# Kernel tuning notes

Hardware: AMD Instinct MI355X
Metric: run time of the kernel (lower is better)

Reference implementation:

```python
import jax, jax.numpy as jnp
import numpy as np

IOU_THRESHOLD = 0.5  # default in ObjectUtils.nms
N_BOXES = 10000


def setup_inputs() -> dict:
    key = jax.random.key(0)
    k1, k2 = jax.random.split(key)
    boxes = jax.random.uniform(k1, (N_BOXES, 4), dtype=jnp.float32)  # normalized cxcywh
    scores = jax.random.uniform(k2, (N_BOXES,), dtype=jnp.float32)
    return {"boxes_cxcywh": boxes, "scores": scores}


def _cxcywh_to_ltrb(b):
    cx, cy, w, h = b[:, 0], b[:, 1], b[:, 2], b[:, 3]
    return jnp.stack([cx - w / 2, cy - h / 2, cx + w / 2, cy + h / 2], axis=1)


def _pairwise_iou(a, b):
    # a: [N1,4] ltrb, b: [N2,4] ltrb -> [N1,N2] (matches ObjectUtils.compute_iou)
    lt = jnp.maximum(a[:, None, :2], b[None, :, :2])
    rb = jnp.minimum(a[:, None, 2:], b[None, :, 2:])
    wh = jnp.clip(rb - lt, 0.0)
    inter = wh[..., 0] * wh[..., 1]
    area_a = (a[:, 2] - a[:, 0]) * (a[:, 3] - a[:, 1])
    area_b = (b[:, 2] - b[:, 0]) * (b[:, 3] - b[:, 1])
    return inter / (area_a[:, None] + area_b[None, :] - inter)


def reference(boxes_cxcywh, scores):
    ltrb = _cxcywh_to_ltrb(boxes_cxcywh)
    iou = _pairwise_iou(ltrb, ltrb)  # [N,N]

    # ---- greedy NMS, faithful to ObjectUtils.nms (unclamped intersection,
    # retain when iou < threshold) expressed as a jit-friendly suppression loop ----
    n = ltrb.shape[0]
    order = jnp.argsort(-scores)  # highest score first (torch.sort ascending, pop last)
    bs = ltrb[order]
    l, t, r, b = bs[:, 0], bs[:, 1], bs[:, 2], bs[:, 3]
    area = (r - l) * (b - t)
    inter_nms = (jnp.minimum(r[:, None], r[None, :]) - jnp.maximum(l[:, None], l[None, :])) * \
                (jnp.minimum(b[:, None], b[None, :]) - jnp.maximum(t[:, None], t[None, :]))
    iou_nms = inter_nms / (area[:, None] + area[None, :] - inter_nms)
    ar = jnp.arange(n)

    def body(i, keep):
        # box i (in sorted order) suppresses lower-scored boxes only if it is itself kept
        suppress = keep[i] & (iou_nms[i] >= IOU_THRESHOLD) & (ar > i)
        return keep & jnp.logical_not(suppress)

    keep_sorted = jax.lax.fori_loop(0, n, body, jnp.ones((n,), dtype=bool))
    keep = jnp.zeros((n,), dtype=bool).at[order].set(keep_sorted)
    return iou, keep
```

## Files before the change

kernel.cpp:

```cpp
#include <hip/hip_runtime.h>

typedef unsigned long long u64;

#define THR 0.5f

__device__ __forceinline__ void conv_box(const float4 b, float& l, float& t,
                                         float& r, float& bo, float& a) {
  #pragma clang fp contract(off)
  float hw = 0.5f * b.z;
  float hh = 0.5f * b.w;
  l = b.x - hw;
  t = b.y - hh;
  r = b.x + hw;
  bo = b.y + hh;
  a = (r - l) * (bo - t);
}

__global__ void k_zero(int* __restrict__ rank, int n) {
  int i = blockIdx.x * blockDim.x + threadIdx.x;
  if (i < n) rank[i] = 0;
}

__global__ void k_rank(const float* __restrict__ scores, int* __restrict__ rank,
                       int n, int jchunk) {
  int i = blockIdx.x * blockDim.x + threadIdx.x;
  if (i >= n) return;
  float si = scores[i];
  int j0 = blockIdx.y * jchunk;
  int j1 = min(j0 + jchunk, n);
  int c = 0;
  for (int j = j0; j < j1; ++j) {
    float sj = scores[j];
    c += ((sj > si) || (sj == si && j < i)) ? 1 : 0;
  }
  if (c) atomicAdd(rank + i, c);
}

__global__ void k_scatter(const float4* __restrict__ boxes, const int* __restrict__ rank,
                          float* __restrict__ sl, float* __restrict__ st,
                          float* __restrict__ sr, float* __restrict__ sb,
                          float* __restrict__ sa, int* __restrict__ sidx, int n) {
  int i = blockIdx.x * blockDim.x + threadIdx.x;
  if (i >= n) return;
  float l, t, r, b, a;
  conv_box(boxes[i], l, t, r, b, a);
  int k = rank[i];
  sl[k] = l; st[k] = t; sr[k] = r; sb[k] = b; sa[k] = a; sidx[k] = i;
}

__global__ void k_mask(const float* __restrict__ sl, const float* __restrict__ st,
                       const float* __restrict__ sr, const float* __restrict__ sb,
                       const float* __restrict__ sa,
                       u64* __restrict__ mask, u64* __restrict__ diag,
                       u64* __restrict__ band, int n, int wstride) {
  #pragma clang fp contract(off)
  int k = blockIdx.x * blockDim.x + threadIdx.x;
  if (k >= n) return;
  int w = blockIdx.y;
  int jbase = w << 6;
  u64 word = 0;
  if (jbase + 63 > k) {
    float l = sl[k], t = st[k], r = sr[k], b = sb[k], a = sa[k];
    int jend = min(jbase + 64, n);
    for (int j = max(jbase, k + 1); j < jend; ++j) {
      float lmax = fmaxf(l, sl[j]);
      float tmax = fmaxf(t, st[j]);
      float rmin = fminf(r, sr[j]);
      float bmin = fminf(b, sb[j]);
      float wd = rmin - lmax;
      float hd = bmin - tmax;
      float inter = wd * hd;
      float denom = (a + sa[j]) - inter;
      float q = inter / denom;
      if (q >= THR) word |= 1ull << (j - jbase);
    }
  }
  mask[(size_t)k * wstride + w] = word;
  int kg = k >> 6;
  if (kg == w) diag[k] = word;
  if (w == kg + 1) band[k] = word;
}

__device__ __forceinline__ void scan_body6(
    const u64* __restrict__ mask, const u64* __restrict__ diag,
    const u64* __restrict__ band, const int* __restrict__ sidx,
    float* __restrict__ keep, int n, int wstride,
    u64* rem, u64* dsh, u64* bsh, int (*kept)[64], int* nk_sh) {
  int t = threadIdx.x, wv = t >> 6, lane = t & 63;
  int ng = (n + 63) >> 6;
  rem[t] = 0;
  if (t < 2) nk_sh[t] = 0;
  int scur = 0;
  u64 bnd = 0;
  if (wv == 0) {
    dsh[lane] = diag[lane];
    bsh[lane] = band[lane];
    if (lane < n) scur = sidx[lane];
  }
  __syncthreads();
  for (int g = 0; g < ng; ++g) {
    int base = g << 6;
    if (wv == 0) {
      int nxt = base + 64 + lane;
      u64 dnext = (g + 1 < ng) ? diag[nxt] : 0;
      u64 bnext = (g + 1 < ng) ? band[nxt] : 0;
      int snew = (g + 1 < ng && nxt < n) ? sidx[nxt] : 0;
      u64 s = rem[g] | bnd;
      int valid = n - base;
      if (valid < 64) s |= (~0ull) << valid;
      u64 kw = 0;
      #pragma unroll
      for (int c = 0; c < 8; ++c) {
        int b0 = c << 3;
        u64 e0 = dsh[b0 + 0], e1 = dsh[b0 + 1], e2 = dsh[b0 + 2], e3 = dsh[b0 + 3];
        u64 e4 = dsh[b0 + 4], e5 = dsh[b0 + 5], e6 = dsh[b0 + 6], e7 = dsh[b0 + 7];
        if ((unsigned)((s >> b0) & 0xFFull) != 0xFFu) {
          #define STEP(Q, EQ) if (!((s >> (b0 + Q)) & 1ull)) { kw |= 1ull << (b0 + Q); s |= EQ; }
          STEP(0, e0) STEP(1, e1) STEP(2, e2) STEP(3, e3)
          STEP(4, e4) STEP(5, e5) STEP(6, e6) STEP(7, e7)
          #undef STEP
        }
      }
      if (base + lane < n)
        keep[scur] = ((kw >> lane) & 1ull) ? 1.0f : 0.0f;
      int nk = __popcll(kw);
      if ((kw >> lane) & 1ull) {
        int pos = __popcll(kw & ((1ull << lane) - 1ull));
        kept[g & 1][pos] = lane;
      }
      int npad = (nk + 15) & ~15;
      if (lane >= nk && lane < npad) kept[g & 1][lane] = 0;
      if (lane == 0) nk_sh[g & 1] = nk;
      u64 bv = ((kw >> lane) & 1ull) ? bsh[lane] : 0ull;
      bv |= __shfl_xor(bv, 32);
      bv |= __shfl_xor(bv, 16);
      bv |= __shfl_xor(bv, 8);
      bv |= __shfl_xor(bv, 4);
      bv |= __shfl_xor(bv, 2);
      bv |= __shfl_xor(bv, 1);
      bnd = bv;
      dsh[lane] = dnext;
      bsh[lane] = bnext;
      scur = snew;
    } else {
      int w = t - 64;
      int gp = g - 1;
      if (gp >= 0 && w > g && w < ng) {
        int nkp = nk_sh[gp & 1];
        if (nkp) {
          const int* kp = kept[gp & 1];
          int basep = gp << 6;
          u64 acc = 0;
          for (int i = 0; i < nkp; i += 16) {
            int k0 = kp[i+0],  k1 = kp[i+1],  k2 = kp[i+2],  k3 = kp[i+3];
            int k4 = kp[i+4],  k5 = kp[i+5],  k6 = kp[i+6],  k7 = kp[i+7];
            int k8 = kp[i+8],  k9 = kp[i+9],  k10 = kp[i+10], k11 = kp[i+11];
            int k12 = kp[i+12], k13 = kp[i+13], k14 = kp[i+14], k15 = kp[i+15];
            u64 v0 = mask[(size_t)(basep + k0) * wstride + w];
            u64 v1 = mask[(size_t)(basep + k1) * wstride + w];
            u64 v2 = mask[(size_t)(basep + k2) * wstride + w];
            u64 v3 = mask[(size_t)(basep + k3) * wstride + w];
            u64 v4 = mask[(size_t)(basep + k4) * wstride + w];
            u64 v5 = mask[(size_t)(basep + k5) * wstride + w];
            u64 v6 = mask[(size_t)(basep + k6) * wstride + w];
            u64 v7 = mask[(size_t)(basep + k7) * wstride + w];
            u64 v8 = mask[(size_t)(basep + k8) * wstride + w];
            u64 v9 = mask[(size_t)(basep + k9) * wstride + w];
            u64 v10 = mask[(size_t)(basep + k10) * wstride + w];
            u64 v11 = mask[(size_t)(basep + k11) * wstride + w];
            u64 v12 = mask[(size_t)(basep + k12) * wstride + w];
            u64 v13 = mask[(size_t)(basep + k13) * wstride + w];
            u64 v14 = mask[(size_t)(basep + k14) * wstride + w];
            u64 v15 = mask[(size_t)(basep + k15) * wstride + w];
            acc |= v0;
            if (i + 1 < nkp)  acc |= v1;
            if (i + 2 < nkp)  acc |= v2;
            if (i + 3 < nkp)  acc |= v3;
            if (i + 4 < nkp)  acc |= v4;
            if (i + 5 < nkp)  acc |= v5;
            if (i + 6 < nkp)  acc |= v6;
            if (i + 7 < nkp)  acc |= v7;
            if (i + 8 < nkp)  acc |= v8;
            if (i + 9 < nkp)  acc |= v9;
            if (i + 10 < nkp) acc |= v10;
            if (i + 11 < nkp) acc |= v11;
            if (i + 12 < nkp) acc |= v12;
            if (i + 13 < nkp) acc |= v13;
            if (i + 14 < nkp) acc |= v14;
            if (i + 15 < nkp) acc |= v15;
          }
          rem[w] |= acc;
        }
      }
    }
    __syncthreads();
  }
}

__global__ __launch_bounds__(256, 1) void k_scan2(const u64* __restrict__ mask,
                                                  const u64* __restrict__ diag,
                                                  const u64* __restrict__ band,
                                                  const int* __restrict__ sidx,
                                                  float* __restrict__ keep,
                                                  int n, int wstride) {
  __shared__ u64 rem[256];
  __shared__ u64 dsh[64];
  __shared__ u64 bsh[64];
  __shared__ int kept[2][64];
  __shared__ int nk_sh[2];
  scan_body6(mask, diag, band, sidx, keep, n, wstride, rem, dsh, bsh, kept, nk_sh);
}

__device__ __forceinline__ float iou_one(float li, float ti, float ri, float bi, float ai,
                                         float lj, float tj, float rj, float bj, float aj) {
  float lmax = fmaxf(li, lj);
  float tmax = fmaxf(ti, tj);
  float rmin = fminf(ri, rj);
  float bmin = fminf(bi, bj);
  float w = fmaxf(rmin - lmax, 0.0f);
  float h = fmaxf(bmin - tmax, 0.0f);
  float inter = w * h;
  float denom = (ai + aj) - inter;
  return inter * __builtin_amdgcn_rcpf(denom);
}

__device__ __forceinline__ void iou_body(const float4* __restrict__ boxes,
                                         float* __restrict__ out,
                                         int n, int rpb, int bx, int by) {
  int nj4 = (n + 3) >> 2;
  int j4 = bx * 256 + threadIdx.x;
  if (j4 >= nj4) return;
  int j = j4 << 2;
  int jc1 = min(j + 1, n - 1), jc2 = min(j + 2, n - 1), jc3 = min(j + 3, n - 1);
  float l0,t0,r0,b0,a0, l1,t1,r1,b1,a1, l2,t2,r2,b2,a2, l3,t3,r3,b3,a3;
  conv_box(boxes[j],   l0,t0,r0,b0,a0);
  conv_box(boxes[jc1], l1,t1,r1,b1,a1);
  conv_box(boxes[jc2], l2,t2,r2,b2,a2);
  conv_box(boxes[jc3], l3,t3,r3,b3,a3);
  bool full = (j + 3) < n;
  for (int rr = 0; rr < rpb; ++rr) {
    int i = by * rpb + rr;
    if (i >= n) return;
    float li,ti,ri,bi,ai;
    conv_box(boxes[i], li,ti,ri,bi,ai);
    float4 o;
    o.x = iou_one(li,ti,ri,bi,ai, l0,t0,r0,b0,a0);
    o.y = iou_one(li,ti,ri,bi,ai, l1,t1,r1,b1,a1);
    o.z = iou_one(li,ti,ri,bi,ai, l2,t2,r2,b2,a2);
    o.w = iou_one(li,ti,ri,bi,ai, l3,t3,r3,b3,a3);
    size_t row = (size_t)i * n;
    if (full) {
      *reinterpret_cast<float4*>(out + row + j) = o;
    } else {
      out[row + j] = o.x;
      if (j + 1 < n) out[row + j + 1] = o.y;
      if (j + 2 < n) out[row + j + 2] = o.z;
    }
  }
}

__global__ void k_iou(const float4* __restrict__ boxes, float* __restrict__ out,
                      int n, int rpb) {
  iou_body(boxes, out, n, rpb, blockIdx.x, blockIdx.y);
}

__global__ __launch_bounds__(256) void k_fused(const float4* __restrict__ boxes,
                                               float* __restrict__ out,
                                               const u64* __restrict__ mask,
                                               const u64* __restrict__ diag,
                                               const u64* __restrict__ band,
                                               const int* __restrict__ sidx,
                                               float* __restrict__ keep,
                                               int n, int wstride, int rpb, int gx) {
  __shared__ u64 rem[256];
  __shared__ u64 dsh[64];
  __shared__ u64 bsh[64];
  __shared__ int kept[2][64];
  __shared__ int nk_sh[2];
  if (blockIdx.x == 0) {
    scan_body6(mask, diag, band, sidx, keep, n, wstride, rem, dsh, bsh, kept, nk_sh);
    return;
  }
  int id = blockIdx.x - 1;
  iou_body(boxes, out, n, rpb, id % gx, id / gx);
}

extern "C" void kernel_launch(void* const* d_in, const int* in_sizes, int n_in,
                              void* d_out, int out_size, void* d_ws, size_t ws_size,
                              hipStream_t stream) {
  const float* boxes = (const float*)d_in[0];
  const float* scores = (const float*)d_in[1];
  int n = in_sizes[1];
  float* out = (float*)d_out;
  size_t NN = (size_t)n * (size_t)n;
  float* keep = out + NN;

  int words = (n + 63) >> 6;
  int wstride = (words + 3) & ~3;
  size_t need = (size_t)n * wstride * 8
              + (size_t)words * 64 * 8 * 2
              + 256
              + (size_t)n * 4 * 7;
  bool use_ws = (ws_size >= need);

  char* base = use_ws ? (char*)d_ws : (char*)d_out;
  size_t off = 0;
  u64* mask = (u64*)(base + off); off += (size_t)n * wstride * 8;
  u64* diag = (u64*)(base + off); off += (size_t)words * 64 * 8;
  u64* band = (u64*)(base + off); off += (size_t)words * 64 * 8;
  off = (off + 255) & ~(size_t)255;
  float* sl  = (float*)(base + off); off += (size_t)n * 4;
  float* st_ = (float*)(base + off); off += (size_t)n * 4;
  float* sr  = (float*)(base + off); off += (size_t)n * 4;
  float* sb  = (float*)(base + off); off += (size_t)n * 4;
  float* sa  = (float*)(base + off); off += (size_t)n * 4;
  int* sidx  = (int*)(base + off); off += (size_t)n * 4;
  int* rank  = (int*)(base + off); off += (size_t)n * 4;

  int nb = (n + 255) / 256;
  k_zero<<<nb, 256, 0, stream>>>(rank, n);

  int jblocks = 40;
  int jchunk = (n + jblocks - 1) / jblocks;
  k_rank<<<dim3(nb, jblocks), 256, 0, stream>>>(scores, rank, n, jchunk);

  k_scatter<<<nb, 256, 0, stream>>>((const float4*)boxes, rank, sl, st_, sr, sb, sa, sidx, n);

  k_mask<<<dim3(nb, words), 256, 0, stream>>>(sl, st_, sr, sb, sa, mask, diag, band, n, wstride);

  int rpb = 10;
  int nj4 = (n + 3) >> 2;
  int gx = (nj4 + 255) / 256;
  int gy = (n + rpb - 1) / rpb;

  if (use_ws) {
    k_fused<<<gx * gy + 1, 256, 0, stream>>>((const float4*)boxes, out, mask, diag,
                                             band, sidx, keep, n, wstride, rpb, gx);
  } else {
    k_scan2<<<1, 256, 0, stream>>>(mask, diag, band, sidx, keep, n, wstride);
    k_iou<<<dim3(gx, gy), 256, 0, stream>>>((const float4*)boxes, out, n, rpb);
  }
}
```

Before: 383.2 us.

## Fuse rank/scatter kernels and streamline serial NMS scan inner loop

Merges the zero, rank and scatter kernels into a single kernel that counts rank over float4-vectorised scores without atomics, which removes two launches but leaves only 40 blocks each doing a full 10000-element sweep. The serial scan now preloads diagonal words from LDS into registers with double buffering, replaces the shuffle OR-reduction with DPP row operations plus readlane, and defers the keep-flag writes to a parallel pass at the end using a shared kwords array. The fused kernel also gets a launch bound hint of 4 blocks per CU. The kwords array is fixed at 160 entries, which caps n at 10240.

After: 717.2 us. +87.2%, slower.

```diff
diff --git a/kernel.cpp b/kernel.cpp
--- a/kernel.cpp
+++ b/kernel.cpp
@@ -16,36 +16,32 @@
   a = (r - l) * (bo - t);
 }
 
-__global__ void k_zero(int* __restrict__ rank, int n) {
-  int i = blockIdx.x * blockDim.x + threadIdx.x;
-  if (i < n) rank[i] = 0;
-}
-
-__global__ void k_rank(const float* __restrict__ scores, int* __restrict__ rank,
-                       int n, int jchunk) {
+__global__ void k_rankscatter(const float4* __restrict__ boxes,
+                              const float* __restrict__ scores,
+                              float* __restrict__ sl, float* __restrict__ st,
+                              float* __restrict__ sr, float* __restrict__ sb,
+                              float* __restrict__ sa, int* __restrict__ sidx, int n) {
   int i = blockIdx.x * blockDim.x + threadIdx.x;
   if (i >= n) return;
   float si = scores[i];
-  int j0 = blockIdx.y * jchunk;
-  int j1 = min(j0 + jchunk, n);
+  const float4* s4 = (const float4*)scores;
+  int n4 = n >> 2;
   int c = 0;
-  for (int j = j0; j < j1; ++j) {
+  for (int j4 = 0; j4 < n4; ++j4) {
+    float4 v = s4[j4];
+    int j = j4 << 2;
+    c += (v.x > si || (v.x == si && j + 0 < i)) ? 1 : 0;
+    c += (v.y > si || (v.y == si && j + 1 < i)) ? 1 : 0;
+    c += (v.z > si || (v.z == si && j + 2 < i)) ? 1 : 0;
+    c += (v.w > si || (v.w == si && j + 3 < i)) ? 1 : 0;
+  }
+  for (int j = n4 << 2; j < n; ++j) {
     float sj = scores[j];
-    c += ((sj > si) || (sj == si && j < i)) ? 1 : 0;
-  }
-  if (c) atomicAdd(rank + i, c);
-}
-
-__global__ void k_scatter(const float4* __restrict__ boxes, const int* __restrict__ rank,
-                          float* __restrict__ sl, float* __restrict__ st,
-                          float* __restrict__ sr, float* __restrict__ sb,
-                          float* __restrict__ sa, int* __restrict__ sidx, int n) {
-  int i = blockIdx.x * blockDim.x + threadIdx.x;
-  if (i >= n) return;
+    c += (sj > si || (sj == si && j < i)) ? 1 : 0;
+  }
   float l, t, r, b, a;
   conv_box(boxes[i], l, t, r, b, a);
-  int k = rank[i];
-  sl[k] = l; st[k] = t; sr[k] = r; sb[k] = b; sa[k] = a; sidx[k] = i;
+  sl[c] = l; st[c] = t; sr[c] = r; sb[c] = b; sa[c] = a; sidx[c] = i;
 }
 
 __global__ void k_mask(const float* __restrict__ sl, const float* __restrict__ st,
@@ -81,21 +77,40 @@
   if (w == kg + 1) band[k] = word;
 }
 
-__device__ __forceinline__ void scan_body6(
+__device__ __forceinline__ u64 wave_or_u64(u64 v) {
+  unsigned lo = (unsigned)v, hi = (unsigned)(v >> 32);
+#define DPP_OR(x, ctrl, rmask) \
+  x |= (unsigned)__builtin_amdgcn_update_dpp(0, (int)(x), ctrl, rmask, 0xF, true)
+  DPP_OR(lo, 0x111, 0xF); DPP_OR(hi, 0x111, 0xF);
+  DPP_OR(lo, 0x112, 0xF); DPP_OR(hi, 0x112, 0xF);
+  DPP_OR(lo, 0x114, 0xF); DPP_OR(hi, 0x114, 0xF);
+  DPP_OR(lo, 0x118, 0xF); DPP_OR(hi, 0x118, 0xF);
+  DPP_OR(lo, 0x142, 0xA); DPP_OR(hi, 0x142, 0xA);
+  DPP_OR(lo, 0x143, 0xC); DPP_OR(hi, 0x143, 0xC);
+#undef DPP_OR
+  unsigned flo = (unsigned)__builtin_amdgcn_readlane((int)lo, 63);
+  unsigned fhi = (unsigned)__builtin_amdgcn_readlane((int)hi, 63);
+  return ((u64)fhi << 32) | flo;
+}
+
+__device__ __forceinline__ void scan_body7(
     const u64* __restrict__ mask, const u64* __restrict__ diag,
     const u64* __restrict__ band, const int* __restrict__ sidx,
     float* __restrict__ keep, int n, int wstride,
-    u64* rem, u64* dsh, u64* bsh, int (*kept)[64], int* nk_sh) {
+    u64* rem, u64* dsh, u64* bsh, u64* kwords, int (*kept)[64], int* nk_sh) {
   int t = threadIdx.x, wv = t >> 6, lane = t & 63;
   int ng = (n + 63) >> 6;
   rem[t] = 0;
   if (t < 2) nk_sh[t] = 0;
-  int scur = 0;
   u64 bnd = 0;
+  u64 x0 = 0, x1 = 0, x2 = 0, x3 = 0, x4 = 0, x5 = 0, x6 = 0, x7 = 0;
+  const ulonglong2* d2 = (const ulonglong2*)dsh;
   if (wv == 0) {
     dsh[lane] = diag[lane];
     bsh[lane] = band[lane];
-    if (lane < n) scur = sidx[lane];
+    ulonglong2 p0 = d2[0], p1 = d2[1], p2 = d2[2], p3 = d2[3];
+    x0 = p0.x; x1 = p0.y; x2 = p1.x; x3 = p1.y;
+    x4 = p2.x; x5 = p2.y; x6 = p3.x; x7 = p3.y;
   }
   __syncthreads();
   for (int g = 0; g < ng; ++g) {
@@ -104,25 +119,32 @@
       int nxt = base + 64 + lane;
       u64 dnext = (g + 1 < ng) ? diag[nxt] : 0;
       u64 bnext = (g + 1 < ng) ? band[nxt] : 0;
-      int snew = (g + 1 < ng && nxt < n) ? sidx[nxt] : 0;
+      u64 bshv = bsh[lane];
       u64 s = rem[g] | bnd;
       int valid = n - base;
       if (valid < 64) s |= (~0ull) << valid;
       u64 kw = 0;
-      #pragma unroll
-      for (int c = 0; c < 8; ++c) {
-        int b0 = c << 3;
-        u64 e0 = dsh[b0 + 0], e1 = dsh[b0 + 1], e2 = dsh[b0 + 2], e3 = dsh[b0 + 3];
-        u64 e4 = dsh[b0 + 4], e5 = dsh[b0 + 5], e6 = dsh[b0 + 6], e7 = dsh[b0 + 7];
-        if ((unsigned)((s >> b0) & 0xFFull) != 0xFFu) {
-          #define STEP(Q, EQ) if (!((s >> (b0 + Q)) & 1ull)) { kw |= 1ull << (b0 + Q); s |= EQ; }
-          STEP(0, e0) STEP(1, e1) STEP(2, e2) STEP(3, e3)
-          STEP(4, e4) STEP(5, e5) STEP(6, e6) STEP(7, e7)
-          #undef STEP
-        }
-      }
-      if (base + lane < n)
-        keep[scur] = ((kw >> lane) & 1ull) ? 1.0f : 0.0f;
+      u64 y0, y1, y2, y3, y4, y5, y6, y7;
+#define LDC(a0,a1,a2,a3,a4,a5,a6,a7, c) { \
+      ulonglong2 q0 = d2[4*(c)], q1 = d2[4*(c)+1], q2 = d2[4*(c)+2], q3 = d2[4*(c)+3]; \
+      a0 = q0.x; a1 = q0.y; a2 = q1.x; a3 = q1.y; a4 = q2.x; a5 = q2.y; a6 = q3.x; a7 = q3.y; }
+#define STEP(BB, EQ) if (!((s >> (BB)) & 1ull)) { kw |= 1ull << (BB); s |= EQ; }
+#define CHUNK(b0v, a0,a1,a2,a3,a4,a5,a6,a7) \
+      if ((unsigned)((s >> (b0v)) & 0xFFull) != 0xFFu) { \
+        STEP(b0v+0, a0) STEP(b0v+1, a1) STEP(b0v+2, a2) STEP(b0v+3, a3) \
+        STEP(b0v+4, a4) STEP(b0v+5, a5) STEP(b0v+6, a6) STEP(b0v+7, a7) }
+      LDC(y0,y1,y2,y3,y4,y5,y6,y7, 1); CHUNK(0,  x0,x1,x2,x3,x4,x5,x6,x7);
+      LDC(x0,x1,x2,x3,x4,x5,x6,x7, 2); CHUNK(8,  y0,y1,y2,y3,y4,y5,y6,y7);
+      LDC(y0,y1,y2,y3,y4,y5,y6,y7, 3); CHUNK(16, x0,x1,x2,x3,x4,x5,x6,x7);
+      LDC(x0,x1,x2,x3,x4,x5,x6,x7, 4); CHUNK(24, y0,y1,y2,y3,y4,y5,y6,y7);
+      LDC(y0,y1,y2,y3,y4,y5,y6,y7, 5); CHUNK(32, x0,x1,x2,x3,x4,x5,x6,x7);
+      LDC(x0,x1,x2,x3,x4,x5,x6,x7, 6); CHUNK(40, y0,y1,y2,y3,y4,y5,y6,y7);
+      LDC(y0,y1,y2,y3,y4,y5,y6,y7, 7); CHUNK(48, x0,x1,x2,x3,x4,x5,x6,x7);
+                                       CHUNK(56, y0,y1,y2,y3,y4,y5,y6,y7);
+#undef CHUNK
+#undef STEP
+#undef LDC
+      if (lane == 0) kwords[g] = kw;
       int nk = __popcll(kw);
       if ((kw >> lane) & 1ull) {
         int pos = __popcll(kw & ((1ull << lane) - 1ull));
@@ -131,17 +153,13 @@
       int npad = (nk + 15) & ~15;
       if (lane >= nk && lane < npad) kept[g & 1][lane] = 0;
       if (lane == 0) nk_sh[g & 1] = nk;
-      u64 bv = ((kw >> lane) & 1ull) ? bsh[lane] : 0ull;
-      bv |= __shfl_xor(bv, 32);
-      bv |= __shfl_xor(bv, 16);
-      bv |= __shfl_xor(bv, 8);
-      bv |= __shfl_xor(bv, 4);
-      bv |= __shfl_xor(bv, 2);
-      bv |= __shfl_xor(bv, 1);
-      bnd = bv;
+      u64 bv = ((kw >> lane) & 1ull) ? bshv : 0ull;
+      bnd = wave_or_u64(bv);
       dsh[lane] = dnext;
       bsh[lane] = bnext;
-      scur = snew;
+      ulonglong2 p0 = d2[0], p1 = d2[1], p2 = d2[2], p3 = d2[3];
+      x0 = p0.x; x1 = p0.y; x2 = p1.x; x3 = p1.y;
+      x4 = p2.x; x5 = p2.y; x6 = p3.x; x7 = p3.y;
     } else {
       int w = t - 64;
       int gp = g - 1;
@@ -195,6 +213,10 @@
     }
     __syncthreads();
   }
+  for (int k = t; k < n; k += 256) {
+    u64 kwv = kwords[k >> 6];
+    keep[sidx[k]] = ((kwv >> (k & 63)) & 1ull) ? 1.0f : 0.0f;
+  }
 }
 
 __global__ __launch_bounds__(256, 1) void k_scan2(const u64* __restrict__ mask,
@@ -204,11 +226,12 @@
                                                   float* __restrict__ keep,
                                                   int n, int wstride) {
   __shared__ u64 rem[256];
-  __shared__ u64 dsh[64];
+  __shared__ __align__(16) u64 dsh[64];
   __shared__ u64 bsh[64];
+  __shared__ u64 kwords[160];
   __shared__ int kept[2][64];
   __shared__ int nk_sh[2];
-  scan_body6(mask, diag, band, sidx, keep, n, wstride, rem, dsh, bsh, kept, nk_sh);
+  scan_body7(mask, diag, band, sidx, keep, n, wstride, rem, dsh, bsh, kwords, kept, nk_sh);
 }
 
 __device__ __forceinline__ float iou_one(float li, float ti, float ri, float bi, float ai,
@@ -264,21 +287,22 @@
   iou_body(boxes, out, n, rpb, blockIdx.x, blockIdx.y);
 }
 
-__global__ __launch_bounds__(256) void k_fused(const float4* __restrict__ boxes,
-                                               float* __restrict__ out,
-                                               const u64* __restrict__ mask,
-                                               const u64* __restrict__ diag,
-                                               const u64* __restrict__ band,
-                                               const int* __restrict__ sidx,
-                                               float* __restrict__ keep,
-                                               int n, int wstride, int rpb, int gx) {
+__global__ __launch_bounds__(256, 4) void k_fused(const float4* __restrict__ boxes,
+                                                  float* __restrict__ out,
+                                                  const u64* __restrict__ mask,
+                                                  const u64* __restrict__ diag,
+                                                  const u64* __restrict__ band,
+                                                  const int* __restrict__ sidx,
+                                                  float* __restrict__ keep,
+                                                  int n, int wstride, int rpb, int gx) {
   __shared__ u64 rem[256];
-  __shared__ u64 dsh[64];
+  __shared__ __align__(16) u64 dsh[64];
   __shared__ u64 bsh[64];
+  __shared__ u64 kwords[160];
   __shared__ int kept[2][64];
   __shared__ int nk_sh[2];
   if (blockIdx.x == 0) {
-    scan_body6(mask, diag, band, sidx, keep, n, wstride, rem, dsh, bsh, kept, nk_sh);
+    scan_body7(mask, diag, band, sidx, keep, n, wstride, rem, dsh, bsh, kwords, kept, nk_sh);
     return;
   }
   int id = blockIdx.x - 1;
@@ -300,7 +324,7 @@
   size_t need = (size_t)n * wstride * 8
               + (size_t)words * 64 * 8 * 2
               + 256
-              + (size_t)n * 4 * 7;
+              + (size_t)n * 4 * 6;
   bool use_ws = (ws_size >= need);
 
   char* base = use_ws ? (char*)d_ws : (char*)d_out;
@@ -315,16 +339,10 @@
   float* sb  = (float*)(base + off); off += (size_t)n * 4;
   float* sa  = (float*)(base + off); off += (size_t)n * 4;
   int* sidx  = (int*)(base + off); off += (size_t)n * 4;
-  int* rank  = (int*)(base + off); off += (size_t)n * 4;
 
   int nb = (n + 255) / 256;
-  k_zero<<<nb, 256, 0, stream>>>(rank, n);
-
-  int jblocks = 40;
-  int jchunk = (n + jblocks - 1) / jblocks;
-  k_rank<<<dim3(nb, jblocks), 256, 0, stream>>>(scores, rank, n, jchunk);
-
-  k_scatter<<<nb, 256, 0, stream>>>((const float4*)boxes, rank, sl, st_, sr, sb, sa, sidx, n);
+  k_rankscatter<<<nb, 256, 0, stream>>>((const float4*)boxes, scores,
+                                        sl, st_, sr, sb, sa, sidx, n);
 
   k_mask<<<dim3(nb, words), 256, 0, stream>>>(sl, st_, sr, sb, sa, mask, diag, band, n, wstride);
 
```
